# Performance work log

Measured on AMD Instinct MI355X. Metric: run time of the kernel, lower is better.

Reference implementation:

```python
import jax, jax.numpy as jnp
import numpy as np

B, J, C = 4096, 17, 512       # batch, joints (length), channels (dim)
K, TOK, CH, H, KS, G = 3, 64, 1024, 8, 3, 8  # adj kernels, tokens_dim, channels_dim, heads, conv_large, gn groups
EPS = 1e-5


def setup_inputs() -> dict:
    key = jax.random.key(0)
    ks = jax.random.split(key, 16)
    r = lambda i, shp, s=0.02: jax.random.normal(ks[i], shp, jnp.float32) * s
    return {
        "x": jax.random.normal(ks[0], (B, J, C), jnp.float32),
        "adj": jax.random.uniform(ks[1], (K, J, J), jnp.float32) / J,
        "norm1_w": jnp.ones((J,), jnp.float32), "norm1_b": jnp.zeros((J,), jnp.float32),
        "gcn1_w": r(2, (K * C, C)), "gcn1_b": jnp.zeros((K * C,), jnp.float32),
        "dw_w": r(3, (C, 1, KS), 0.1), "dw_b": jnp.zeros((C,), jnp.float32),
        "gn1_w": jnp.ones((C,), jnp.float32), "gn1_b": jnp.zeros((C,), jnp.float32),
        "pw_w": r(4, (C, C)), "pw_b": jnp.zeros((C,), jnp.float32),
        "mlp1_w1": r(5, (TOK, J)), "mlp1_b1": jnp.zeros((TOK,), jnp.float32),
        "mlp1_w2": r(6, (J, TOK)), "mlp1_b2": jnp.zeros((J,), jnp.float32),
        "qkv_w": r(7, (3 * C, C)), "qkv_b": jnp.zeros((3 * C,), jnp.float32),
        "proj_w": r(8, (C, C)), "proj_b": jnp.zeros((C,), jnp.float32),
        "gnf_w": jnp.ones((C,), jnp.float32), "gnf_b": jnp.zeros((C,), jnp.float32),
        "norm2_w": jnp.ones((C,), jnp.float32), "norm2_b": jnp.zeros((C,), jnp.float32),
        "mlp2_w1": r(9, (CH, C)), "mlp2_b1": jnp.zeros((CH,), jnp.float32),
        "mlp2_w2": r(10, (C, CH)), "mlp2_b2": jnp.zeros((C,), jnp.float32),
        "gcn2_w": r(11, (K * C, C)), "gcn2_b": jnp.zeros((K * C,), jnp.float32),
    }


def _gelu(t):
    return jax.nn.gelu(t, approximate=False)  # torch nn.GELU default is exact erf


def _ln(t, w, b):  # LayerNorm over last axis
    m = t.mean(-1, keepdims=True)
    v = ((t - m) ** 2).mean(-1, keepdims=True)
    return (t - m) * jax.lax.rsqrt(v + EPS) * w + b


def _gn(t, w, b):  # GroupNorm(G, C) over (B, C, J)
    Bn, Cc, Jn = t.shape
    r = t.reshape(Bn, G, -1)
    m = r.mean(-1, keepdims=True)
    v = ((r - m) ** 2).mean(-1, keepdims=True)
    r = (r - m) * jax.lax.rsqrt(v + EPS)
    return r.reshape(Bn, Cc, Jn) * w[:, None] + b[:, None]


def _gcn(t, w, b, adj):  # t: (B,C,J); 1x1 conv to K*C then einsum with adj (K,J,J)
    y = jnp.einsum('bcj,oc->boj', t, w) + b[:, None]
    y = y.reshape(t.shape[0], K, C, t.shape[2])
    return jnp.einsum('bkcv,kvw->bcw', y, adj)


def reference(x, adj, norm1_w, norm1_b, gcn1_w, gcn1_b, dw_w, dw_b, gn1_w, gn1_b,
              pw_w, pw_b, mlp1_w1, mlp1_b1, mlp1_w2, mlp1_b2, qkv_w, qkv_b,
              proj_w, proj_b, gnf_w, gnf_b, norm2_w, norm2_b,
              mlp2_w1, mlp2_b1, mlp2_w2, mlp2_b2, gcn2_w, gcn2_b):
    res = x                                   # (B,J,C)
    xc = jnp.swapaxes(x, 1, 2)                # (B,C,J)
    xc = _ln(xc, norm1_w, norm1_b)            # LayerNorm over joints

    # --- branch 1: GCN ---
    x_gcn1 = _gcn(xc, gcn1_w, gcn1_b, adj)    # (B,C,J)

    # --- branch 2: depthwise conv + token MLP ---
    h = jax.lax.conv_general_dilated(xc, dw_w, (1,), [(KS // 2, KS // 2)],
                                     dimension_numbers=('NCH', 'OIH', 'NCH'),
                                     feature_group_count=C) + dw_b[:, None]
    h = _gelu(_gn(h, gn1_w, gn1_b))
    h = jnp.einsum('bcj,oc->boj', h, pw_w) + pw_b[:, None]      # 1x1 conv
    h = _gelu(jnp.einsum('bcj,tj->bct', h, mlp1_w1) + mlp1_b1)  # token mlp fc1
    h = jnp.einsum('bct,jt->bcj', h, mlp1_w2) + mlp1_b2         # token mlp fc2

    # --- branch 3: global spatial attention over joints ---
    dh = C // H
    qkv = jnp.einsum('bcj,oc->boj', xc, qkv_w) + qkv_b[:, None]  # (B,3C,J)
    q, k_, v_ = jnp.split(qkv, 3, axis=1)
    q = q.reshape(-1, H, dh, J); k_ = k_.reshape(-1, H, dh, J); v_ = v_.reshape(-1, H, dh, J)
    attn = jax.nn.softmax(jnp.einsum('bhdi,bhdj->bhij', q, k_) / jnp.sqrt(jnp.float32(dh)), axis=-1)
    sga = jnp.einsum('bhij,bhdj->bhdi', attn, v_).reshape(-1, C, J)
    sga = jnp.einsum('bcj,oc->boj', sga, proj_w) + proj_b[:, None]

    # --- fuse ---
    xc = _gelu(_gn(sga + x_gcn1 + h, gnf_w, gnf_b))
    xj = jnp.swapaxes(xc, 1, 2)               # (B,J,C)
    res_channel = xj
    xn = _ln(xj + res, norm2_w, norm2_b)      # LayerNorm over channels
    m = _gelu(jnp.einsum('bjc,hc->bjh', xn, mlp2_w1) + mlp2_b1)
    m = jnp.einsum('bjh,ch->bjc', m, mlp2_w2) + mlp2_b2
    g2 = _gcn(jnp.swapaxes(m, 1, 2), gcn2_w, gcn2_b, adj)  # (B,C,J)
    xj = res_channel + jnp.swapaxes(g2, 1, 2)
    return xj + res
```

## Files before the change

kernel.cpp:

```cpp
#include <hip/hip_runtime.h>
#include <stdint.h>

#define BB 4096
#define JJ 17
#define CC 512

typedef unsigned short u16;
typedef __bf16 bf16x8 __attribute__((ext_vector_type(8)));
typedef float  f32x4  __attribute__((ext_vector_type(4)));
typedef float  f32x2  __attribute__((ext_vector_type(2)));

__device__ __forceinline__ float bf2f(u16 u){ return __uint_as_float(((uint32_t)u)<<16); }
__device__ __forceinline__ u16 f2bf(float f){
  uint32_t u = __float_as_uint(f);
  u += 0x7fffu + ((u>>16)&1u);
  return (u16)(u>>16);
}
__device__ __forceinline__ void unpk2(uint32_t u, float& lo, float& hi){
  lo = __uint_as_float(u<<16);
  hi = __uint_as_float(u & 0xffff0000u);
}
__device__ __forceinline__ float gelu_f(float x){
  float x2 = x*x;
  float y2 = x*fmaf(0.0713548162726f, x2, 1.59576912161f);
  float ey = __builtin_amdgcn_exp2f(y2*1.44269504089f);
  return fmaf(-x, __builtin_amdgcn_rcpf(ey+1.f), x);
}
__device__ __forceinline__ void pkfma(f32x2& d, f32x2 a, f32x2 b){
  asm volatile("v_pk_fma_f32 %0, %1, %2, %0" : "+v"(d) : "v"(a), "v"(b));
}
__device__ __forceinline__ void gll16(const void* g, void* l){
  __builtin_amdgcn_global_load_lds(
      (const __attribute__((address_space(1))) void*)g,
      (__attribute__((address_space(3))) void*)l, 16, 0, 0);
}

__global__ void k_cvt(const float* __restrict__ in, u16* __restrict__ out, int n){
  int i = blockIdx.x*blockDim.x + threadIdx.x;
  if (i < n) out[i] = f2bf(in[i]);
}

__global__ void k_tokprep(const float* __restrict__ w1, const float* __restrict__ w2,
                          float* __restrict__ w1p, float* __restrict__ w2p){
  int i = blockIdx.x*blockDim.x + threadIdx.x;
  if (i >= 1280) return;
  int t = i/20, j = i%20;
  w1p[i] = (j<17) ? w1[t*17+j] : 0.f;
  w2p[i] = (j<17) ? w2[j*64+t] : 0.f;
}

__global__ __launch_bounds__(512) void k_pre(
    const float* __restrict__ x, int b0,
    const float* __restrict__ n1w, const float* __restrict__ n1b,
    const float* __restrict__ dww, const float* __restrict__ dwb,
    const float* __restrict__ gn1w, const float* __restrict__ gn1b,
    u16* __restrict__ xc, u16* __restrict__ hgn)
{
  int b = blockIdx.x, c = threadIdx.x;
  const float* xp = x + (size_t)(b0+b)*JJ*CC + c;
  float v[JJ]; float s = 0.f;
  #pragma unroll
  for (int j=0;j<JJ;j++){ v[j] = xp[(size_t)j*CC]; s += v[j]; }
  float mn = s*(1.f/JJ); float var = 0.f;
  #pragma unroll
  for (int j=0;j<JJ;j++){ float d=v[j]-mn; var += d*d; }
  float rr = rsqrtf(var*(1.f/JJ)+1e-5f);
  float xcv[JJ];
  #pragma unroll
  for (int j=0;j<JJ;j++) xcv[j] = (v[j]-mn)*rr*n1w[j] + n1b[j];
  u16* xo = xc + (size_t)b*JJ*CC + c;
  #pragma unroll
  for (int j=0;j<JJ;j++) xo[(size_t)j*CC] = f2bf(xcv[j]);
  float w0=dww[c*3+0], w1=dww[c*3+1], w2=dww[c*3+2], db=dwb[c];
  float h[JJ];
  #pragma unroll
  for (int j=0;j<JJ;j++){
    float a = db + w1*xcv[j];
    if (j>0)    a += w0*xcv[j-1];
    if (j<JJ-1) a += w2*xcv[j+1];
    h[j] = a;
  }
  float ss=0.f, sq=0.f;
  #pragma unroll
  for (int j=0;j<JJ;j++){ ss += h[j]; sq += h[j]*h[j]; }
  for (int off=32; off; off>>=1){ ss += __shfl_xor(ss,off); sq += __shfl_xor(sq,off); }
  float gm = ss*(1.f/(64.f*JJ));
  float gr = rsqrtf(sq*(1.f/(64.f*JJ)) - gm*gm + 1e-5f);
  float gw = gn1w[c], gb = gn1b[c];
  u16* ho = hgn + (size_t)b*JJ*CC + c;
  #pragma unroll
  for (int j=0;j<JJ;j++){
    float t = (h[j]-gm)*gr*gw + gb;
    ho[(size_t)j*CC] = f2bf(gelu_f(t));
  }
}

template<int DO_GELU, int DO_ADD>
__global__ __launch_bounds__(256,3) void gemm_r3(
    const u16* __restrict__ A, const u16* __restrict__ W, const float* __restrict__ bias,
    u16* __restrict__ out, const u16* __restrict__ add0, const u16* __restrict__ add1,
    int M, int N, int K, int NXT)
{
  __shared__ __align__(16) u16 lds[24576];
  const int tid = threadIdx.x;
  const int wid = tid>>6, lane = tid&63;

  const int nwg = gridDim.x;
  const int q8 = nwg>>3, r8 = nwg&7;
  const int xcd = blockIdx.x & 7, sub = blockIdx.x >> 3;
  const int wg = (xcd<r8 ? xcd*(q8+1) : r8*(q8+1)+(xcd-r8)*q8) + sub;
  const int n0 = (wg % NXT)*128;
  const int m0 = (wg / NXT)*128;

  const int wm = wid>>1, wn = wid&1;
  const int lr = lane&15, lg = lane>>4;
  const int T  = K>>5;

  const int srow = tid>>2;
  const int gswS = ((tid&3) ^ ((tid>>3)&3))<<3;
  const u16* gA = A + (size_t)(m0+srow)*K + gswS;
  const u16* gB = W + (size_t)(n0+srow)*K + gswS;
  const int K64 = K<<6;
  const int dstl = tid*8;

  const int g8 = (lg ^ ((lr>>1)&3))<<3;
  const int offA0 = (wm*64+lr)*32 + g8;
  const int offB0 = 4096 + (wn*64+lr)*32 + g8;

  f32x4 acc[4][4];
  #pragma unroll
  for (int i=0;i<4;i++)
    #pragma unroll
    for (int j=0;j<4;j++) acc[i][j] = (f32x4){0.f,0.f,0.f,0.f};

  auto STAGE = [&](int t, int sofs){
    const u16* ga = gA + t*32;
    const u16* gb = gB + t*32;
    u16* la = lds + sofs + dstl;
    u16* lb = lds + sofs + 4096 + dstl;
    gll16(ga,     la);
    gll16(ga+K64, la+2048);
    gll16(gb,     lb);
    gll16(gb+K64, lb+2048);
  };

  STAGE(0, 0); STAGE(1, 8192);
  asm volatile("s_waitcnt vmcnt(4)" ::: "memory");
  __builtin_amdgcn_s_barrier();

  int s0 = 0, s1 = 8192, s2 = 16384;
  for (int t=0; t<T; ++t){
    const bool more = (t+2 < T);
    if (more) STAGE(t+2, s2);
    bf16x8 av[4], bv[4];
    #pragma unroll
    for (int i=0;i<4;i++) av[i] = *(const bf16x8*)&lds[s0 + offA0 + i*512];
    #pragma unroll
    for (int j=0;j<4;j++) bv[j] = *(const bf16x8*)&lds[s0 + offB0 + j*512];
    asm volatile("s_waitcnt lgkmcnt(0)" ::: "memory");
    __builtin_amdgcn_sched_barrier(0);
    __builtin_amdgcn_s_setprio(1);
    #pragma unroll
    for (int i=0;i<4;i++)
      #pragma unroll
      for (int j=0;j<4;j++)
        acc[i][j] = __builtin_amdgcn_mfma_f32_16x16x32_bf16(av[i], bv[j], acc[i][j], 0,0,0);
    __builtin_amdgcn_s_setprio(0);
    if (more) asm volatile("s_waitcnt vmcnt(4)" ::: "memory");
    else      asm volatile("s_waitcnt vmcnt(0)" ::: "memory");
    __builtin_amdgcn_s_barrier();
    const int tmp = s0; s0 = s1; s1 = s2; s2 = tmp;
  }

  const int rbase = lg*4;
  #pragma unroll
  for (int i=0;i<4;i++){
    #pragma unroll
    for (int j=0;j<4;j++){
      const int col  = n0 + wn*64 + j*16 + lr;
      const int row0 = m0 + wm*64 + i*16 + rbase;
      const float bvl = bias[col];
      #pragma unroll
      for (int r=0;r<4;r++){
        size_t idx = (size_t)(row0+r)*N + col;
        float v = acc[i][j][r] + bvl;
        if (DO_ADD)  v += bf2f(add0[idx]) + bf2f(add1[idx]);
        if (DO_GELU) v = gelu_f(v);
        out[idx] = f2bf(v);
      }
    }
  }
}

template<int FINAL>
__global__ __launch_bounds__(512) void k_gcn2(
    const u16* __restrict__ G, const float* __restrict__ adj,
    u16* __restrict__ xg,
    const u16* __restrict__ rc, const float* __restrict__ x, int b0,
    float* __restrict__ out)
{
  __shared__ __align__(16) float adjp[51*20];
  const int tid = threadIdx.x;
  for (int i=tid; i<1020; i+=512){
    int r=i/20, cl=i%20;
    adjp[i] = (cl<17) ? adj[r*17+cl] : 0.f;
  }
  __syncthreads();

  const int sl  = tid>>7;
  const int l   = tid&127;
  const int c0  = l*4;
  const int bl  = blockIdx.x*4 + sl;

  float acc[JJ][4];
  #pragma unroll
  for (int w=0;w<JJ;w++)
    #pragma unroll
    for (int e=0;e<4;e++) acc[w][e]=0.f;

  const u16* gbase = G + (size_t)bl*JJ*1536 + c0;
  #pragma unroll 3
  for (int kv=0; kv<51; kv++){
    const int k = kv/JJ, v = kv - k*JJ;
    uint2 yu = *(const uint2*)(gbase + (size_t)v*1536 + k*512);
    float y0,y1,y2,y3;
    unpk2(yu.x, y0, y1);
    unpk2(yu.y, y2, y3);
    const f32x4* arow = (const f32x4*)&adjp[kv*20];
    f32x4 a0=arow[0], a1=arow[1], a2=arow[2], a3=arow[3];
    float a16 = adjp[kv*20+16];
    float ar[JJ] = {a0[0],a0[1],a0[2],a0[3], a1[0],a1[1],a1[2],a1[3],
                    a2[0],a2[1],a2[2],a2[3], a3[0],a3[1],a3[2],a3[3], a16};
    #pragma unroll
    for (int w=0;w<JJ;w++){
      acc[w][0] += y0*ar[w];
      acc[w][1] += y1*ar[w];
      acc[w][2] += y2*ar[w];
      acc[w][3] += y3*ar[w];
    }
  }

  if (FINAL==0){
    u16* xo = xg + (size_t)bl*JJ*CC + c0;
    #pragma unroll
    for (int w=0;w<JJ;w++){
      uint2 o;
      o.x = (uint32_t)f2bf(acc[w][0]) | ((uint32_t)f2bf(acc[w][1])<<16);
      o.y = (uint32_t)f2bf(acc[w][2]) | ((uint32_t)f2bf(acc[w][3])<<16);
      *(uint2*)(xo + (size_t)w*CC) = o;
    }
  } else {
    const size_t gb = (size_t)(b0+bl)*JJ*CC + c0;
    const u16* rp = rc + (size_t)bl*JJ*CC + c0;
    #pragma unroll
    for (int w=0;w<JJ;w++){
      uint2 ru = *(const uint2*)(rp + (size_t)w*CC);
      float r0,r1,r2,r3;
      unpk2(ru.x, r0, r1);
      unpk2(ru.y, r2, r3);
      f32x4 xv = *(const f32x4*)(x + gb + (size_t)w*CC);
      f32x4 o;
      o[0]=acc[w][0]+r0+xv[0]; o[1]=acc[w][1]+r1+xv[1];
      o[2]=acc[w][2]+r2+xv[2]; o[3]=acc[w][3]+r3+xv[3];
      *(f32x4*)(out + gb + (size_t)w*CC) = o;
    }
  }
}

__global__ __launch_bounds__(512) void k_attn(const u16* __restrict__ Gqkv, u16* __restrict__ sga){
  __shared__ __align__(16) u16 qs[8*17*72];
  __shared__ __align__(16) u16 ks_[8*17*72];
  __shared__ __align__(16) float at[8*17*20];
  int b = blockIdx.x, tid = threadIdx.x;
  int h = tid>>6, d = tid&63;
  const u16* base = Gqkv + (size_t)b*JJ*1536;
  float vv[JJ];
  #pragma unroll
  for (int i=0;i<JJ;i++){
    qs [(h*JJ+i)*72 + d] = base[(size_t)i*1536 +        h*64 + d];
    ks_[(h*JJ+i)*72 + d] = base[(size_t)i*1536 +  512 + h*64 + d];
    vv[i] = bf2f(base[(size_t)i*1536 + 1024 + h*64 + d]);
  }
  __syncthreads();
  for (int p=d; p<289; p+=64){
    int i=p/JJ, j=p-i*JJ;
    const u16* qrow = &qs [(h*JJ+i)*72];
    const u16* krow = &ks_[(h*JJ+j)*72];
    float a=0.f;
    #pragma unroll
    for (int t=0;t<8;t++){
      bf16x8 q8 = *(const bf16x8*)&qrow[t*8];
      bf16x8 k8 = *(const bf16x8*)&krow[t*8];
      #pragma unroll
      for (int e=0;e<8;e++) a += (float)q8[e]*(float)k8[e];
    }
    at[(h*JJ+i)*20 + j] = a*0.125f;
  }
  __syncthreads();
  if (d < JJ){
    float* row = &at[(h*JJ+d)*20];
    f32x4 r0=((f32x4*)row)[0], r1=((f32x4*)row)[1], r2=((f32x4*)row)[2], r3=((f32x4*)row)[3];
    float e16=row[16];
    float rv[JJ]={r0[0],r0[1],r0[2],r0[3],r1[0],r1[1],r1[2],r1[3],
                  r2[0],r2[1],r2[2],r2[3],r3[0],r3[1],r3[2],r3[3],e16};
    float mx=-1e30f;
    #pragma unroll
    for (int j=0;j<JJ;j++) mx=fmaxf(mx,rv[j]);
    float sm=0.f;
    #pragma unroll
    for (int j=0;j<JJ;j++){ rv[j]=__builtin_amdgcn_exp2f((rv[j]-mx)*1.44269504089f); sm+=rv[j]; }
    float inv=1.f/sm;
    #pragma unroll
    for (int j=0;j<JJ;j++) row[j]=rv[j]*inv;
  }
  __syncthreads();
  #pragma unroll
  for (int i=0;i<JJ;i++){
    const float* row = &at[(h*JJ+i)*20];
    f32x4 r0=((const f32x4*)row)[0], r1=((const f32x4*)row)[1],
          r2=((const f32x4*)row)[2], r3=((const f32x4*)row)[3];
    float a = r0[0]*vv[0]+r0[1]*vv[1]+r0[2]*vv[2]+r0[3]*vv[3]
            + r1[0]*vv[4]+r1[1]*vv[5]+r1[2]*vv[6]+r1[3]*vv[7]
            + r2[0]*vv[8]+r2[1]*vv[9]+r2[2]*vv[10]+r2[3]*vv[11]
            + r3[0]*vv[12]+r3[1]*vv[13]+r3[2]*vv[14]+r3[3]*vv[15]
            + row[16]*vv[16];
    sga[((size_t)b*JJ+i)*CC + h*64 + d] = f2bf(a);
  }
}

__global__ __launch_bounds__(512) void k_tok(const u16* __restrict__ Hpw,
    const float* __restrict__ w1p, const float* __restrict__ w2p,
    const float* __restrict__ b1, const float* __restrict__ b2,
    u16* __restrict__ h2o){
  __shared__ __align__(16) float w1s[1280], w2s[1280];
  __shared__ float b1s[64], b2s[20];
  const int tid = threadIdx.x;
  for (int i=tid; i<1280; i+=512){ w1s[i]=w1p[i]; w2s[i]=w2p[i]; }
  if (tid<64) b1s[tid]=b1[tid];
  if (tid<20) b2s[tid] = (tid<17) ? b2[tid] : 0.f;
  __syncthreads();

  const int bl = blockIdx.x*2 + (tid>>8);
  const int c0 = tid&255;
  const u16* hp = Hpw + (size_t)bl*JJ*CC;
  float hv0[JJ], hv1[JJ];
  #pragma unroll
  for (int j=0;j<JJ;j++){
    hv0[j]=bf2f(hp[(size_t)j*CC + c0]);
    hv1[j]=bf2f(hp[(size_t)j*CC + c0 + 256]);
  }
  f32x2 h0p[9], h1p[9];
  #pragma unroll
  for (int p=0;p<8;p++){
    h0p[p] = (f32x2){hv0[2*p], hv0[2*p+1]};
    h1p[p] = (f32x2){hv1[2*p], hv1[2*p+1]};
  }
  h0p[8] = (f32x2){hv0[16], 0.f};
  h1p[8] = (f32x2){hv1[16], 0.f};

  f32x2 a20[9], a21[9];
  #pragma unroll
  for (int p=0;p<9;p++){
    f32x2 bb = (f32x2){b2s[2*p], b2s[2*p+1]};
    a20[p]=bb; a21[p]=bb;
  }

  for (int t=0;t<64;t++){
    f32x4 wa = *(const f32x4*)&w1s[t*20];
    f32x4 wb = *(const f32x4*)&w1s[t*20+4];
    f32x4 wc = *(const f32x4*)&w1s[t*20+8];
    f32x4 wd = *(const f32x4*)&w1s[t*20+12];
    float  we = w1s[t*20+16];
    f32x2 wp[9] = {(f32x2){wa[0],wa[1]},(f32x2){wa[2],wa[3]},
                   (f32x2){wb[0],wb[1]},(f32x2){wb[2],wb[3]},
                   (f32x2){wc[0],wc[1]},(f32x2){wc[2],wc[3]},
                   (f32x2){wd[0],wd[1]},(f32x2){wd[2],wd[3]},
                   (f32x2){we,0.f}};
    f32x2 s0 = (f32x2){b1s[t], 0.f};
    f32x2 s1 = s0;
    #pragma unroll
    for (int p=0;p<9;p++){ pkfma(s0, h0p[p], wp[p]); pkfma(s1, h1p[p], wp[p]); }
    float a0 = gelu_f(s0[0] + s0[1]);
    float a1 = gelu_f(s1[0] + s1[1]);
    wa = *(const f32x4*)&w2s[t*20];
    wb = *(const f32x4*)&w2s[t*20+4];
    wc = *(const f32x4*)&w2s[t*20+8];
    wd = *(const f32x4*)&w2s[t*20+12];
    we = w2s[t*20+16];
    f32x2 wq[9] = {(f32x2){wa[0],wa[1]},(f32x2){wa[2],wa[3]},
                   (f32x2){wb[0],wb[1]},(f32x2){wb[2],wb[3]},
                   (f32x2){wc[0],wc[1]},(f32x2){wc[2],wc[3]},
                   (f32x2){wd[0],wd[1]},(f32x2){wd[2],wd[3]},
                   (f32x2){we,0.f}};
    f32x2 a0b = (f32x2){a0,a0};
    f32x2 a1b = (f32x2){a1,a1};
    #pragma unroll
    for (int p=0;p<9;p++){ pkfma(a20[p], a0b, wq[p]); pkfma(a21[p], a1b, wq[p]); }
  }
  u16* ho = h2o + (size_t)bl*JJ*CC;
  #pragma unroll
  for (int j=0;j<JJ;j++){
    ho[(size_t)j*CC + c0]       = f2bf(a20[j>>1][j&1]);
    ho[(size_t)j*CC + c0 + 256] = f2bf(a21[j>>1][j&1]);
  }
}

__global__ __launch_bounds__(512) void k_fuse(const u16* __restrict__ s,
    const float* __restrict__ x, int b0,
    const float* __restrict__ gfw, const float* __restrict__ gfb,
    const float* __restrict__ n2w, const float* __restrict__ n2b,
    u16* __restrict__ rc, u16* __restrict__ xn){
  __shared__ float rS[8][JJ], rQ[8][JJ];
  int b = blockIdx.x, c = threadIdx.x;
  int wave = c>>6, lane = c&63;
  const u16* sp = s + (size_t)b*JJ*CC + c;
  float sv[JJ];
  #pragma unroll
  for (int j=0;j<JJ;j++) sv[j]=bf2f(sp[(size_t)j*CC]);
  float ss=0.f, sq=0.f;
  #pragma unroll
  for (int j=0;j<JJ;j++){ ss+=sv[j]; sq+=sv[j]*sv[j]; }
  for (int off=32; off; off>>=1){ ss += __shfl_xor(ss,off); sq += __shfl_xor(sq,off); }
  float gm = ss*(1.f/1088.f);
  float gr = rsqrtf(sq*(1.f/1088.f) - gm*gm + 1e-5f);
  float gw=gfw[c], gb=gfb[c];
  const float* xp = x + (size_t)(b0+b)*JJ*CC + c;
  u16* rp = rc + (size_t)b*JJ*CC + c;
  float t[JJ];
  #pragma unroll
  for (int j=0;j<JJ;j++){
    float v = gelu_f((sv[j]-gm)*gr*gw + gb);
    rp[(size_t)j*CC] = f2bf(v);
    t[j] = v + xp[(size_t)j*CC];
  }
  #pragma unroll
  for (int j=0;j<JJ;j++){
    float a=t[j], q=a*a;
    for (int off=32; off; off>>=1){ a+=__shfl_xor(a,off); q+=__shfl_xor(q,off); }
    if (lane==0){ rS[wave][j]=a; rQ[wave][j]=q; }
  }
  __syncthreads();
  float wN=n2w[c], bN=n2b[c];
  u16* xo = xn + (size_t)b*JJ*CC + c;
  #pragma unroll
  for (int j=0;j<JJ;j++){
    float S=0.f,Q=0.f;
    #pragma unroll
    for (int w=0;w<8;w++){ S+=rS[w][j]; Q+=rQ[w][j]; }
    float mn=S*(1.f/512.f);
    float r2=rsqrtf(Q*(1.f/512.f)-mn*mn+1e-5f);
    xo[(size_t)j*CC]=f2bf((t[j]-mn)*r2*wN+bN);
  }
}

extern "C" void kernel_launch(void* const* d_in, const int* in_sizes, int n_in,
                              void* d_out, int out_size, void* d_ws, size_t ws_size,
                              hipStream_t stream)
{
  const float* x      = (const float*)d_in[0];
  const float* adj    = (const float*)d_in[1];
  const float* n1w    = (const float*)d_in[2];
  const float* n1b    = (const float*)d_in[3];
  const float* gcn1_w = (const float*)d_in[4];
  const float* gcn1_b = (const float*)d_in[5];
  const float* dw_w   = (const float*)d_in[6];
  const float* dw_b   = (const float*)d_in[7];
  const float* gn1_w  = (const float*)d_in[8];
  const float* gn1_b  = (const float*)d_in[9];
  const float* pw_w   = (const float*)d_in[10];
  const float* pw_b   = (const float*)d_in[11];
  const float* m1w1   = (const float*)d_in[12];
  const float* m1b1   = (const float*)d_in[13];
  const float* m1w2   = (const float*)d_in[14];
  const float* m1b2   = (const float*)d_in[15];
  const float* qkv_w  = (const float*)d_in[16];
  const float* qkv_b  = (const float*)d_in[17];
  const float* proj_w = (const float*)d_in[18];
  const float* proj_b = (const float*)d_in[19];
  const float* gnf_w  = (const float*)d_in[20];
  const float* gnf_b  = (const float*)d_in[21];
  const float* n2w    = (const float*)d_in[22];
  const float* n2b    = (const float*)d_in[23];
  const float* m2w1   = (const float*)d_in[24];
  const float* m2b1   = (const float*)d_in[25];
  const float* m2w2   = (const float*)d_in[26];
  const float* m2b2   = (const float*)d_in[27];
  const float* gcn2_w = (const float*)d_in[28];
  const float* gcn2_b = (const float*)d_in[29];
  float* out = (float*)d_out;

  char* ws = (char*)d_ws;
  const size_t WBYTES = (size_t)3932160*2;
  const size_t TPBYTES = 2560*4;

  const int cands[5] = {4096,2048,1024,512,256};
  int NB = 0;
  for (int ci=0; ci<5; ci++){
    size_t need = WBYTES + TPBYTES + (size_t)cands[ci]*JJ*2*(1536 + 4*512);
    if (need <= ws_size){ NB = cands[ci]; break; }
  }
  if (NB == 0) return;

  u16* wb = (u16*)ws;
  float* w1p = (float*)(ws + WBYTES);
  float* w2p = w1p + 1280;
  char* p = ws + WBYTES + TPBYTES;
  const size_t SZ_BIGc = (size_t)NB*JJ*1536*2;
  const size_t SZTc    = (size_t)NB*JJ*512*2;
  u16* big = (u16*)p;               p += SZ_BIGc;
  u16* t0  = (u16*)p;               p += SZTc;
  u16* t1  = (u16*)p;               p += SZTc;
  u16* t2  = (u16*)p;               p += SZTc;
  u16* t3  = (u16*)p;

  u16 *wg1=wb, *wqkv=wb+786432, *wpw=wb+1572864, *wproj=wb+1835008,
      *wm1=wb+2097152, *wm2=wb+2621440, *wg2=wb+3145728;

  k_cvt<<<(786432+255)/256,256,0,stream>>>(gcn1_w,wg1,786432);
  k_cvt<<<(786432+255)/256,256,0,stream>>>(qkv_w,wqkv,786432);
  k_cvt<<<(262144+255)/256,256,0,stream>>>(pw_w,wpw,262144);
  k_cvt<<<(262144+255)/256,256,0,stream>>>(proj_w,wproj,262144);
  k_cvt<<<(524288+255)/256,256,0,stream>>>(m2w1,wm1,524288);
  k_cvt<<<(524288+255)/256,256,0,stream>>>(m2w2,wm2,524288);
  k_cvt<<<(786432+255)/256,256,0,stream>>>(gcn2_w,wg2,786432);
  k_tokprep<<<5,256,0,stream>>>(m1w1,m1w2,w1p,w2p);

  const int M2 = NB*JJ;
  const int MT = M2/128;
  for (int b0 = 0; b0 < BB; b0 += NB){
    k_pre<<<NB,512,0,stream>>>(x,b0,n1w,n1b,dw_w,dw_b,gn1_w,gn1_b, t0, t1);
    gemm_r3<0,0><<<MT*12,256,0,stream>>>(t0,wg1,gcn1_b,big,nullptr,nullptr,M2,1536,512,12);
    k_gcn2<0><<<NB/4,512,0,stream>>>(big,adj,t2,nullptr,nullptr,0,nullptr);
    gemm_r3<0,0><<<MT*12,256,0,stream>>>(t0,wqkv,qkv_b,big,nullptr,nullptr,M2,1536,512,12);
    k_attn<<<NB,512,0,stream>>>(big,t3);
    gemm_r3<0,0><<<MT*4,256,0,stream>>>(t1,wpw,pw_b,t0,nullptr,nullptr,M2,512,512,4);
    k_tok<<<NB/2,512,0,stream>>>(t0,w1p,w2p,m1b1,m1b2,t1);
    gemm_r3<0,1><<<MT*4,256,0,stream>>>(t3,wproj,proj_b,t0,t2,t1,M2,512,512,4);
    k_fuse<<<NB,512,0,stream>>>(t0,x,b0,gnf_w,gnf_b,n2w,n2b,t1,t2);
    gemm_r3<1,0><<<MT*8,256,0,stream>>>(t2,wm1,m2b1,big,nullptr,nullptr,M2,1024,512,8);
    gemm_r3<0,0><<<MT*4,256,0,stream>>>(big,wm2,m2b2,t0,nullptr,nullptr,M2,512,1024,4);
    gemm_r3<0,0><<<MT*12,256,0,stream>>>(t0,wg2,gcn2_b,big,nullptr,nullptr,M2,1536,512,12);
    k_gcn2<1><<<NB/4,512,0,stream>>>(big,adj,nullptr,t1,x,b0,out);
  }
}
```

Baseline: 1.420 ms.

## Enlarge GEMM tiles to 256x256 with 512-thread workgroups

Replaces the 128x128 tile GEMM run by 256 threads with a 256x256 tile run by 512 threads. Each wave now computes a 128x64 sub-tile with 32 accumulators, and LDS grows to 96KB for the triple-buffered stages. The aim is higher arithmetic intensity and fewer global loads per FLOP. In exchange, occupancy drops to one workgroup per CU and there are fewer workgroups, so tail and wave-quantization effects may grow. It also removes the explicit lgkmcnt wait before the MFMAs and relies on the compiler to insert it.

```diff
diff --git a/kernel.cpp b/kernel.cpp
--- a/kernel.cpp
+++ b/kernel.cpp
@@ -96,12 +96,12 @@
 }
 
 template<int DO_GELU, int DO_ADD>
-__global__ __launch_bounds__(256,3) void gemm_r3(
+__global__ __launch_bounds__(512,1) void gemm_w(
     const u16* __restrict__ A, const u16* __restrict__ W, const float* __restrict__ bias,
     u16* __restrict__ out, const u16* __restrict__ add0, const u16* __restrict__ add1,
     int M, int N, int K, int NXT)
 {
-  __shared__ __align__(16) u16 lds[24576];
+  __shared__ __align__(16) u16 lds[49152];
   const int tid = threadIdx.x;
   const int wid = tid>>6, lane = tid&63;
 
@@ -109,10 +109,10 @@
   const int q8 = nwg>>3, r8 = nwg&7;
   const int xcd = blockIdx.x & 7, sub = blockIdx.x >> 3;
   const int wg = (xcd<r8 ? xcd*(q8+1) : r8*(q8+1)+(xcd-r8)*q8) + sub;
-  const int n0 = (wg % NXT)*128;
-  const int m0 = (wg / NXT)*128;
-
-  const int wm = wid>>1, wn = wid&1;
+  const int n0 = (wg % NXT)*256;
+  const int m0 = (wg / NXT)*256;
+
+  const int wm = wid>>2, wn = wid&3;
   const int lr = lane&15, lg = lane>>4;
   const int T  = K>>5;
 
@@ -120,48 +120,46 @@
   const int gswS = ((tid&3) ^ ((tid>>3)&3))<<3;
   const u16* gA = A + (size_t)(m0+srow)*K + gswS;
   const u16* gB = W + (size_t)(n0+srow)*K + gswS;
-  const int K64 = K<<6;
+  const int K128 = K<<7;
   const int dstl = tid*8;
 
   const int g8 = (lg ^ ((lr>>1)&3))<<3;
-  const int offA0 = (wm*64+lr)*32 + g8;
-  const int offB0 = 4096 + (wn*64+lr)*32 + g8;
-
-  f32x4 acc[4][4];
-  #pragma unroll
-  for (int i=0;i<4;i++)
+  const int offA = (wm*128+lr)*32 + g8;
+  const int offB = 8192 + (wn*64+lr)*32 + g8;
+
+  f32x4 acc[8][4];
+  #pragma unroll
+  for (int i=0;i<8;i++)
     #pragma unroll
     for (int j=0;j<4;j++) acc[i][j] = (f32x4){0.f,0.f,0.f,0.f};
 
   auto STAGE = [&](int t, int sofs){
     const u16* ga = gA + t*32;
     const u16* gb = gB + t*32;
-    u16* la = lds + sofs + dstl;
-    u16* lb = lds + sofs + 4096 + dstl;
-    gll16(ga,     la);
-    gll16(ga+K64, la+2048);
-    gll16(gb,     lb);
-    gll16(gb+K64, lb+2048);
+    u16* l = lds + sofs + dstl;
+    gll16(ga,       l);
+    gll16(ga+K128,  l+4096);
+    gll16(gb,       l+8192);
+    gll16(gb+K128,  l+12288);
   };
 
-  STAGE(0, 0); STAGE(1, 8192);
+  STAGE(0, 0); STAGE(1, 16384);
   asm volatile("s_waitcnt vmcnt(4)" ::: "memory");
   __builtin_amdgcn_s_barrier();
-
-  int s0 = 0, s1 = 8192, s2 = 16384;
+  __builtin_amdgcn_sched_barrier(0);
+
+  int s0 = 0, s1 = 16384, s2 = 32768;
   for (int t=0; t<T; ++t){
     const bool more = (t+2 < T);
     if (more) STAGE(t+2, s2);
-    bf16x8 av[4], bv[4];
-    #pragma unroll
-    for (int i=0;i<4;i++) av[i] = *(const bf16x8*)&lds[s0 + offA0 + i*512];
-    #pragma unroll
-    for (int j=0;j<4;j++) bv[j] = *(const bf16x8*)&lds[s0 + offB0 + j*512];
-    asm volatile("s_waitcnt lgkmcnt(0)" ::: "memory");
-    __builtin_amdgcn_sched_barrier(0);
+    bf16x8 av[8], bv[4];
+    #pragma unroll
+    for (int i=0;i<8;i++) av[i] = *(const bf16x8*)&lds[s0 + offA + i*512];
+    #pragma unroll
+    for (int j=0;j<4;j++) bv[j] = *(const bf16x8*)&lds[s0 + offB + j*512];
     __builtin_amdgcn_s_setprio(1);
     #pragma unroll
-    for (int i=0;i<4;i++)
+    for (int i=0;i<8;i++)
       #pragma unroll
       for (int j=0;j<4;j++)
         acc[i][j] = __builtin_amdgcn_mfma_f32_16x16x32_bf16(av[i], bv[j], acc[i][j], 0,0,0);
@@ -169,21 +167,22 @@
     if (more) asm volatile("s_waitcnt vmcnt(4)" ::: "memory");
     else      asm volatile("s_waitcnt vmcnt(0)" ::: "memory");
     __builtin_amdgcn_s_barrier();
+    __builtin_amdgcn_sched_barrier(0);
     const int tmp = s0; s0 = s1; s1 = s2; s2 = tmp;
   }
 
   const int rbase = lg*4;
   #pragma unroll
-  for (int i=0;i<4;i++){
-    #pragma unroll
-    for (int j=0;j<4;j++){
-      const int col  = n0 + wn*64 + j*16 + lr;
-      const int row0 = m0 + wm*64 + i*16 + rbase;
+  for (int mi=0; mi<8; mi++){
+    #pragma unroll
+    for (int ni=0; ni<4; ni++){
+      const int col  = n0 + wn*64 + ni*16 + lr;
+      const int row0 = m0 + wm*128 + mi*16 + rbase;
       const float bvl = bias[col];
       #pragma unroll
       for (int r=0;r<4;r++){
         size_t idx = (size_t)(row0+r)*N + col;
-        float v = acc[i][j][r] + bvl;
+        float v = acc[mi][ni][r] + bvl;
         if (DO_ADD)  v += bf2f(add0[idx]) + bf2f(add1[idx]);
         if (DO_GELU) v = gelu_f(v);
         out[idx] = f2bf(v);
@@ -526,20 +525,20 @@
   k_tokprep<<<5,256,0,stream>>>(m1w1,m1w2,w1p,w2p);
 
   const int M2 = NB*JJ;
-  const int MT = M2/128;
+  const int MT = M2/256;
   for (int b0 = 0; b0 < BB; b0 += NB){
     k_pre<<<NB,512,0,stream>>>(x,b0,n1w,n1b,dw_w,dw_b,gn1_w,gn1_b, t0, t1);
-    gemm_r3<0,0><<<MT*12,256,0,stream>>>(t0,wg1,gcn1_b,big,nullptr,nullptr,M2,1536,512,12);
+    gemm_w<0,0><<<MT*6,512,0,stream>>>(t0,wg1,gcn1_b,big,nullptr,nullptr,M2,1536,512,6);
     k_gcn2<0><<<NB/4,512,0,stream>>>(big,adj,t2,nullptr,nullptr,0,nullptr);
-    gemm_r3<0,0><<<MT*12,256,0,stream>>>(t0,wqkv,qkv_b,big,nullptr,nullptr,M2,1536,512,12);
+    gemm_w<0,0><<<MT*6,512,0,stream>>>(t0,wqkv,qkv_b,big,nullptr,nullptr,M2,1536,512,6);
     k_attn<<<NB,512,0,stream>>>(big,t3);
-    gemm_r3<0,0><<<MT*4,256,0,stream>>>(t1,wpw,pw_b,t0,nullptr,nullptr,M2,512,512,4);
+    gemm_w<0,0><<<MT*2,512,0,stream>>>(t1,wpw,pw_b,t0,nullptr,nullptr,M2,512,512,2);
     k_tok<<<NB/2,512,0,stream>>>(t0,w1p,w2p,m1b1,m1b2,t1);
-    gemm_r3<0,1><<<MT*4,256,0,stream>>>(t3,wproj,proj_b,t0,t2,t1,M2,512,512,4);
+    gemm_w<0,1><<<MT*2,512,0,stream>>>(t3,wproj,proj_b,t0,t2,t1,M2,512,512,2);
     k_fuse<<<NB,512,0,stream>>>(t0,x,b0,gnf_w,gnf_b,n2w,n2b,t1,t2);
-    gemm_r3<1,0><<<MT*8,256,0,stream>>>(t2,wm1,m2b1,big,nullptr,nullptr,M2,1024,512,8);
-    gemm_r3<0,0><<<MT*4,256,0,stream>>>(big,wm2,m2b2,t0,nullptr,nullptr,M2,512,1024,4);
-    gemm_r3<0,0><<<MT*12,256,0,stream>>>(t0,wg2,gcn2_b,big,nullptr,nullptr,M2,1536,512,12);
+    gemm_w<1,0><<<MT*4,512,0,stream>>>(t2,wm1,m2b1,big,nullptr,nullptr,M2,1024,512,4);
+    gemm_w<0,0><<<MT*2,512,0,stream>>>(big,wm2,m2b2,t0,nullptr,nullptr,M2,512,1024,2);
+    gemm_w<0,0><<<MT*6,512,0,stream>>>(t0,wg2,gcn2_b,big,nullptr,nullptr,M2,1536,512,6);
     k_gcn2<1><<<NB/4,512,0,stream>>>(big,adj,nullptr,t1,x,b0,out);
   }
 }
```

After: 1.443 ms. No clear change (+1.6%).
